# Performance work log

Hardware: AMD Instinct MI355X
Metric: run time of the kernel (lower is better)

## Reference

```python
import jax, jax.numpy as jnp
import numpy as np

B, L, D = 2, 2048, 2048
H, G, HD = 16, 4, 128
EPS = 1e-6
THETA_BASE = 10000.0


def setup_inputs() -> dict:
    key = jax.random.key(0)
    ks = jax.random.split(key, 5)
    x = jax.random.normal(ks[0], (B, L, D), jnp.float32)
    Wq = jax.random.normal(ks[1], (D, H * HD), jnp.float32) * 0.02
    Wk = jax.random.normal(ks[2], (D, G * HD), jnp.float32) * 0.02
    Wv = jax.random.normal(ks[3], (D, G * HD), jnp.float32) * 0.02
    Wo = jax.random.normal(ks[4], (H * HD, D), jnp.float32) * 0.02
    q_scale = jnp.ones((HD,), jnp.float32)
    k_scale = jnp.ones((HD,), jnp.float32)
    # Well-formed RoPE tables of shape [L, HD] (duplicated-half layout expected by apply_rope)
    inv_freq = 1.0 / (THETA_BASE ** (jnp.arange(0, HD // 2, dtype=jnp.float32) * 2.0 / HD))  # [HD/2]
    angles = jnp.arange(L, dtype=jnp.float32)[:, None] * inv_freq[None, :]  # [L, HD/2]
    angles = jnp.concatenate([angles, angles], axis=1)  # [L, HD]
    cos = jnp.cos(angles)
    sin = jnp.sin(angles)
    # Causal mask: True = masked (matches masked_fill(mask, -inf))
    mask = jnp.triu(jnp.ones((L, L), dtype=bool), k=1)
    return {"x": x, "Wq": Wq, "Wk": Wk, "Wv": Wv, "Wo": Wo,
            "q_scale": q_scale, "k_scale": k_scale, "cos": cos, "sin": sin, "mask": mask}


def _rmsnorm(x, scale):
    var = jnp.mean(x * x, axis=-1, keepdims=True)
    return x * jax.lax.rsqrt(var + EPS) * scale


def _rope(x, cos, sin):
    # x: [B, h, L, HD]; cos/sin: [L, HD]
    hd = x.shape[-1]
    x1, x2 = x[..., : hd // 2], x[..., hd // 2 :]
    rotated = jnp.concatenate([-x2, x1], axis=-1)
    return x * cos[None, None] + rotated * sin[None, None]


def reference(x, Wq, Wk, Wv, Wo, q_scale, k_scale, cos, sin, mask):
    b, l, _ = x.shape
    q = (x @ Wq).reshape(b, l, H, HD).transpose(0, 2, 1, 3)  # [B,H,L,HD]
    k = (x @ Wk).reshape(b, l, G, HD).transpose(0, 2, 1, 3)  # [B,G,L,HD]
    v = (x @ Wv).reshape(b, l, G, HD).transpose(0, 2, 1, 3)
    q = _rmsnorm(q, q_scale)
    k = _rmsnorm(k, k_scale)
    q = _rope(q, cos, sin)
    k = _rope(k, cos, sin)
    gs = H // G
    k = jnp.repeat(k, gs, axis=1)  # [B,H,L,HD]
    v = jnp.repeat(v, gs, axis=1)
    scores = jnp.einsum('bhqd,bhkd->bhqk', q, k)
    scores = jnp.where(mask, -jnp.inf, scores)
    # NB: faithful to the source's unusual scaling by head_dim**2 (not sqrt)
    w = jax.nn.softmax(scores / float(HD ** 2), axis=-1)
    out = jnp.einsum('bhqk,bhkd->bhqd', w, v).transpose(0, 2, 1, 3).reshape(b, l, H * HD)
    return out @ Wo
```

## Files before the change

kernel.cpp:

```cpp
#include <hip/hip_runtime.h>
#include <math.h>

#define SEQ 2048
#define DMODEL 2048
#define NHQ 16
#define NHK 4

typedef __attribute__((ext_vector_type(8))) short short8;
typedef __attribute__((ext_vector_type(8))) unsigned short ushort8;
typedef __attribute__((ext_vector_type(4))) float floatx4;

#define AS1 __attribute__((address_space(1)))
#define AS3 __attribute__((address_space(3)))

__device__ __forceinline__ unsigned short f2bf(float f) {
  unsigned int u = __builtin_bit_cast(unsigned int, f);
  u += 0x7fffu + ((u >> 16) & 1u);
  return (unsigned short)(u >> 16);
}
__device__ __forceinline__ float bf2f(unsigned short s) {
  unsigned int u = ((unsigned int)s) << 16;
  return __builtin_bit_cast(float, u);
}

__global__ __launch_bounds__(256) void prep(const float* __restrict__ x,
                                            const float* __restrict__ Wq,
                                            const float* __restrict__ Wk,
                                            const float* __restrict__ Wv,
                                            const float* __restrict__ Wo,
                                            unsigned short* __restrict__ x_bf,
                                            unsigned short* __restrict__ wqkv_t,
                                            unsigned short* __restrict__ wo_t) {
  const int z = blockIdx.z;
  const int tx = threadIdx.x, ty = threadIdx.y;
  const int tid = ty * 32 + tx;
  if (z == 3) {
    const size_t base = ((size_t)(blockIdx.y * 64 + blockIdx.x)) * 4096 + (size_t)tid * 16;
    const float4 v0 = *(const float4*)(x + base);
    const float4 v1 = *(const float4*)(x + base + 4);
    const float4 v2 = *(const float4*)(x + base + 8);
    const float4 v3 = *(const float4*)(x + base + 12);
    ushort8 w0, w1;
    w0[0] = f2bf(v0.x); w0[1] = f2bf(v0.y); w0[2] = f2bf(v0.z); w0[3] = f2bf(v0.w);
    w0[4] = f2bf(v1.x); w0[5] = f2bf(v1.y); w0[6] = f2bf(v1.z); w0[7] = f2bf(v1.w);
    w1[0] = f2bf(v2.x); w1[1] = f2bf(v2.y); w1[2] = f2bf(v2.z); w1[3] = f2bf(v2.w);
    w1[4] = f2bf(v3.x); w1[5] = f2bf(v3.y); w1[6] = f2bf(v3.z); w1[7] = f2bf(v3.w);
    *(ushort8*)(x_bf + base) = w0;
    *(ushort8*)(x_bf + base + 8) = w1;
    return;
  }
  int bx = blockIdx.x;
  const float* in;
  unsigned short* out;
  int C;
  const int R = 2048;
  if (z == 0)      { in = Wq; out = wqkv_t;                          C = 2048; }
  else if (z == 1) { in = Wo; out = wo_t;                            C = 2048; }
  else {
    if (bx < 16)      { in = Wk; out = wqkv_t + (size_t)2048 * 2048; C = 512; }
    else if (bx < 32) { in = Wv; out = wqkv_t + (size_t)2560 * 2048; C = 512; bx -= 16; }
    else return;
  }
  __shared__ float tile[32][65];
  const int c0 = bx * 32, r0 = blockIdx.y * 64;
#pragma unroll
  for (int j = 0; j < 8; ++j)
    tile[tx][ty + j * 8] = in[(size_t)(r0 + ty + j * 8) * C + c0 + tx];
  __syncthreads();
  const int c = tid >> 3;
  const int l8 = tid & 7;
  ushort8 w;
#pragma unroll
  for (int u = 0; u < 8; ++u) w[u] = f2bf(tile[c][l8 * 8 + u]);
  *(ushort8*)(out + (size_t)(c0 + c) * R + r0 + l8 * 8) = w;
}

#define PBAR() do { __builtin_amdgcn_sched_barrier(0); __builtin_amdgcn_s_barrier(); \
                    __builtin_amdgcn_sched_barrier(0); } while (0)
#define KWAIT(deep) do { if (deep) asm volatile("s_waitcnt vmcnt(8)" ::: "memory"); \
                         else      asm volatile("s_waitcnt vmcnt(0)" ::: "memory"); } while (0)

__device__ __forceinline__ void mfma_q(floatx4 (&ac)[4][4],
                                       const short8 (&a)[4], const short8 (&b)[4]) {
#pragma unroll
  for (int i = 0; i < 4; ++i)
#pragma unroll
    for (int j = 0; j < 4; ++j)
      ac[i][j] = __builtin_amdgcn_mfma_f32_16x16x32_bf16(a[i], b[j], ac[i][j], 0, 0, 0);
}

__device__ __forceinline__ void ld4(short8 (&v)[4], const unsigned short* p) {
#pragma unroll
  for (int i = 0; i < 4; ++i) v[i] = *(const short8*)(p + i * 512);
}

__device__ __forceinline__ void stg_half(const unsigned short* src0,
                                         unsigned short* dst_uniform) {
  __builtin_amdgcn_global_load_lds((const AS1 void*)src0,
                                   (AS3 void*)dst_uniform, 16, 0, 0);
  __builtin_amdgcn_global_load_lds((const AS1 void*)(src0 + (size_t)128 * 2048),
                                   (AS3 void*)(dst_uniform + 4096), 16, 0, 0);
}

__device__ __forceinline__ void kloop256(const unsigned short* __restrict__ A,
                                         const unsigned short* __restrict__ Bt,
                                         unsigned short* ldsA, unsigned short* ldsB,
                                         int bm, int bn, int tid,
                                         floatx4 (&accL)[4][4], floatx4 (&accH)[4][4]) {
  const int wave = tid >> 6;
  const int lane = tid & 63;
  const int m15 = lane & 15;
  const int quad = lane >> 4;
  const int wr = wave >> 2;
  const int wcol = wave & 3;

  const int srow = tid >> 2;
  const int csrc = ((tid & 3) ^ (srow & 3)) * 8;
  const unsigned short* gA = A + (size_t)(bm + srow) * 2048 + csrc;
  const unsigned short* gB = Bt + (size_t)(bn + srow) * 2048 + csrc;
  const int wslot = wave * 512;

  const int aoff = (wr * 128 + m15) * 32 + (quad ^ (m15 & 3)) * 8;
  const int boff = (wcol * 64 + m15) * 32 + (quad ^ (m15 & 3)) * 8;

  stg_half(gA + 0,  ldsA + wslot);
  stg_half(gB + 0,  ldsB + wslot);
  stg_half(gA + 32, ldsA + 8192 + wslot);
  stg_half(gB + 32, ldsB + 8192 + wslot);
  stg_half(gA + 64, ldsA + 16384 + wslot);
  stg_half(gB + 64, ldsB + 16384 + wslot);
  asm volatile("s_waitcnt vmcnt(0)" ::: "memory");
  __builtin_amdgcn_s_barrier();
  __builtin_amdgcn_sched_barrier(0);

  const int NK = 32;
  short8 af[4], bv[4];
  for (int t = 0; t < NK; ++t) {
    const int d = t & 1;
    unsigned short* Ab0 = ldsA + d * 16384;
    unsigned short* Bb0 = ldsB + d * 16384;
    unsigned short* Aalt = ldsA + (d ^ 1) * 16384;
    unsigned short* Balt = ldsB + (d ^ 1) * 16384;
    const bool st1 = (t + 1 < NK), st2 = (t + 2 < NK);
    const int k1 = (t + 1) * 64 + 32;
    const int k2 = (t + 2) * 64;

    ld4(af, Ab0 + aoff);
    ld4(bv, Bb0 + boff);
    if (st1) stg_half(gA + k1, Aalt + 8192 + wslot);
    PBAR();
    __builtin_amdgcn_s_setprio(1);
    mfma_q(accL, af, bv);
    __builtin_amdgcn_s_setprio(0);
    PBAR();

    ld4(af, Ab0 + aoff + 2048);
    if (st1) stg_half(gB + k1, Balt + 8192 + wslot);
    PBAR();
    __builtin_amdgcn_s_setprio(1);
    mfma_q(accH, af, bv);
    __builtin_amdgcn_s_setprio(0);
    KWAIT(st2);
    PBAR();

    ld4(af, Ab0 + 8192 + aoff);
    ld4(bv, Bb0 + 8192 + boff);
    if (st2) stg_half(gA + k2, Ab0 + wslot);
    PBAR();
    __builtin_amdgcn_s_setprio(1);
    mfma_q(accL, af, bv);
    __builtin_amdgcn_s_setprio(0);
    PBAR();

    ld4(af, Ab0 + 8192 + aoff + 2048);
    if (st2) stg_half(gB + k2, Bb0 + wslot);
    PBAR();
    __builtin_amdgcn_s_setprio(1);
    mfma_q(accH, af, bv);
    __builtin_amdgcn_s_setprio(0);
    KWAIT(st2);
    PBAR();
  }
}

__global__ __launch_bounds__(512, 2) void gemm_qkv_fused(const unsigned short* __restrict__ A,
                                                         const unsigned short* __restrict__ Bt,
                                                         unsigned short* __restrict__ qout,
                                                         unsigned short* __restrict__ kout,
                                                         unsigned short* __restrict__ vout,
                                                         const float* __restrict__ q_scale,
                                                         const float* __restrict__ k_scale,
                                                         const float* __restrict__ cosb,
                                                         const float* __restrict__ sinb) {
  __shared__ unsigned short lds[65536];
  unsigned short* ldsA = lds;
  unsigned short* ldsB = lds + 32768;

  const int tid = threadIdx.x;
  const int wave = tid >> 6;
  const int lane = tid & 63;
  const int m15 = lane & 15;
  const int quad = lane >> 4;
  const int wr = wave >> 2;
  const int wcol = wave & 3;
  const int bxn = blockIdx.x;
  const int bm = blockIdx.y * 256;
  const int bn = bxn * 256;

  floatx4 accL[4][4], accH[4][4];
#pragma unroll
  for (int i = 0; i < 4; ++i)
#pragma unroll
    for (int j = 0; j < 4; ++j) {
      accL[i][j] = (floatx4){0.f, 0.f, 0.f, 0.f};
      accH[i][j] = (floatx4){0.f, 0.f, 0.f, 0.f};
    }

  kloop256(A, Bt, ldsA, ldsB, bm, bn, tid, accL, accH);

  unsigned short* epi = lds;
  const int b = bm >> 11;
  const int l_base = bm & (SEQ - 1);
  const int t64 = tid & 63;

  for (int c = 0; c < 2; ++c) {
    __syncthreads();
    if ((wcol >> 1) == c) {
      const int colb = (wcol & 1) * 64;
#pragma unroll
      for (int i = 0; i < 4; ++i)
#pragma unroll
        for (int j = 0; j < 4; ++j)
#pragma unroll
          for (int r = 0; r < 4; ++r) {
            epi[(wr * 128 + i * 16 + quad * 4 + r) * 129 + colb + j * 16 + m15] =
                f2bf(accL[i][j][r]);
            epi[(wr * 128 + 64 + i * 16 + quad * 4 + r) * 129 + colb + j * 16 + m15] =
                f2bf(accH[i][j][r]);
          }
    }
    __syncthreads();

    const int hh = 2 * bxn + c;
    if (hh < 20) {
      const float* scale = (hh < NHQ) ? q_scale : k_scale;
      unsigned short* dstbase = (hh < NHQ)
          ? qout + ((size_t)(b * NHQ + hh) * SEQ + l_base) * 128
          : kout + ((size_t)(b * NHK + (hh - NHQ)) * SEQ + l_base) * 128;
      const float sc0 = scale[t64];
      const float sc1 = scale[t64 + 64];
#pragma unroll 4
      for (int rr = 0; rr < 32; ++rr) {
        const int row = wave * 32 + rr;
        const float v0 = bf2f(epi[row * 129 + t64]);
        const float v1 = bf2f(epi[row * 129 + t64 + 64]);
        float ss = v0 * v0 + v1 * v1;
#pragma unroll
        for (int m = 1; m < 64; m <<= 1) ss += __shfl_xor(ss, m);
        const float r = rsqrtf(ss * (1.0f / 128.0f) + 1e-6f);
        const int l = l_base + row;
        const float c0v = cosb[(size_t)l * 128 + t64];
        const float s0 = sinb[(size_t)l * 128 + t64];
        const float c1v = cosb[(size_t)l * 128 + t64 + 64];
        const float s1 = sinb[(size_t)l * 128 + t64 + 64];
        const float a0 = v0 * r * sc0;
        const float a1 = v1 * r * sc1;
        unsigned short* dst = dstbase + (size_t)row * 128;
        dst[t64]      = f2bf(a0 * c0v - a1 * s0);
        dst[t64 + 64] = f2bf(a1 * c1v + a0 * s1);
      }
    } else {
      const int g = hh - 20;
      unsigned short* vbase = vout + (size_t)(b * NHK + g) * 128 * SEQ + l_base;
#pragma unroll 4
      for (int dd = 0; dd < 16; ++dd) {
        const int d = wave * 16 + dd;
        unsigned short* dst = vbase + (size_t)d * SEQ;
        dst[t64]       = epi[t64 * 129 + d];
        dst[t64 + 64]  = epi[(t64 + 64) * 129 + d];
        dst[t64 + 128] = epi[(t64 + 128) * 129 + d];
        dst[t64 + 192] = epi[(t64 + 192) * 129 + d];
      }
    }
  }
}

__global__ __launch_bounds__(512, 2) void gemm_bf16_f32(const unsigned short* __restrict__ A,
                                                        const unsigned short* __restrict__ Bt,
                                                        float* __restrict__ C,
                                                        int M, int N, int K) {
  __shared__ unsigned short lds[65536];
  unsigned short* ldsA = lds;
  unsigned short* ldsB = lds + 32768;

  const int tid = threadIdx.x;
  const int wave = tid >> 6;
  const int lane = tid & 63;
  const int m15 = lane & 15;
  const int quad = lane >> 4;
  const int wr = wave >> 2;
  const int wcol = wave & 3;
  const int bm = blockIdx.y * 256;
  const int bn = blockIdx.x * 256;

  floatx4 accL[4][4], accH[4][4];
#pragma unroll
  for (int i = 0; i < 4; ++i)
#pragma unroll
    for (int j = 0; j < 4; ++j) {
      accL[i][j] = (floatx4){0.f, 0.f, 0.f, 0.f};
      accH[i][j] = (floatx4){0.f, 0.f, 0.f, 0.f};
    }

  kloop256(A, Bt, ldsA, ldsB, bm, bn, tid, accL, accH);

#pragma unroll
  for (int i = 0; i < 4; ++i)
#pragma unroll
    for (int j = 0; j < 4; ++j)
#pragma unroll
      for (int r = 0; r < 4; ++r) {
        const int col = bn + wcol * 64 + j * 16 + m15;
        C[(size_t)(bm + wr * 128 + i * 16 + quad * 4 + r) * N + col] = accL[i][j][r];
        C[(size_t)(bm + wr * 128 + 64 + i * 16 + quad * 4 + r) * N + col] = accH[i][j][r];
      }
}

__global__ __launch_bounds__(256, 4) void attn_mfma(const unsigned short* __restrict__ qb,
                                                    const unsigned short* __restrict__ kb,
                                                    const unsigned short* __restrict__ vtb,
                                                    unsigned short* __restrict__ o) {
  __shared__ unsigned short Ks[64 * 128];
  __shared__ unsigned short Vs[128 * 64];
  unsigned short* Ps = Ks;

  const int tid = threadIdx.x;
  const int wave = tid >> 6;
  const int lane = tid & 63;
  const int m15 = lane & 15;
  const int quad = lane >> 4;
  const int bh = blockIdx.x;
  const int b = bh >> 4;
  const int h = bh & 15;
  const int g = h >> 2;
  const int q0 = ((int)gridDim.y - 1 - (int)blockIdx.y) * 64;

  const unsigned short* qhead = qb + (size_t)bh * SEQ * 128;
  const unsigned short* khead = kb + (size_t)(b * NHK + g) * SEQ * 128;
  const unsigned short* vthead = vtb + (size_t)(b * NHK + g) * 128 * SEQ;

  short8 qf[4];
  {
    const unsigned short* qp = qhead + (size_t)(q0 + wave * 16 + m15) * 128 + quad * 8;
#pragma unroll
    for (int ks = 0; ks < 4; ++ks) qf[ks] = *(const short8*)(qp + ks * 32);
  }

  floatx4 acc_o[8];
#pragma unroll
  for (int n = 0; n < 8; ++n) acc_o[n] = (floatx4){0.f, 0.f, 0.f, 0.f};
  float l_lane[4] = {0.f, 0.f, 0.f, 0.f};
  const float inv_scale = 1.0f / 16384.0f;

  for (int j0 = 0; j0 <= q0; j0 += 64) {
#pragma unroll
    for (int t = 0; t < 4; ++t) {
      const int r = wave * 16 + t * 4 + (lane >> 4);
      const int cg = (lane & 15) ^ (r & 15);
      const unsigned short* src = khead + (size_t)(j0 + r) * 128 + cg * 8;
      __builtin_amdgcn_global_load_lds(
          (const AS1 void*)src,
          (AS3 void*)&Ks[(wave * 16 + t * 4) * 128], 16, 0, 0);
    }
#pragma unroll
    for (int t = 0; t < 4; ++t) {
      const int d = wave * 32 + t * 8 + (lane >> 3);
      const int cg = (lane & 7) ^ (d & 7);
      const unsigned short* src = vthead + (size_t)d * SEQ + j0 + cg * 8;
      __builtin_amdgcn_global_load_lds(
          (const AS1 void*)src,
          (AS3 void*)&Vs[(wave * 32 + t * 8) * 64], 16, 0, 0);
    }
    __syncthreads();

    floatx4 acc_s[4];
#pragma unroll
    for (int n = 0; n < 4; ++n) acc_s[n] = (floatx4){0.f, 0.f, 0.f, 0.f};
#pragma unroll
    for (int ks = 0; ks < 4; ++ks) {
#pragma unroll
      for (int n = 0; n < 4; ++n) {
        const short8 bfrag = *(const short8*)&Ks[(n * 16 + m15) * 128 + (((ks * 4 + quad) ^ m15) * 8)];
        acc_s[n] = __builtin_amdgcn_mfma_f32_16x16x32_bf16(qf[ks], bfrag, acc_s[n], 0, 0, 0);
      }
    }
    __syncthreads();

    if (j0 == q0) {
      const int row_g = wave * 16 + quad * 4;
#pragma unroll
      for (int n = 0; n < 4; ++n) {
        const int col = n * 16 + m15;
#pragma unroll
        for (int rg = 0; rg < 4; ++rg) {
          float p = (col > row_g + rg) ? 0.0f : __expf(acc_s[n][rg] * inv_scale);
          l_lane[rg] += p;
          Ps[(wave * 16 + quad * 4 + rg) * 72 + n * 16 + m15] = f2bf(p);
        }
      }
    } else {
#pragma unroll
      for (int n = 0; n < 4; ++n) {
#pragma unroll
        for (int rg = 0; rg < 4; ++rg) {
          const float p = __expf(acc_s[n][rg] * inv_scale);
          l_lane[rg] += p;
          Ps[(wave * 16 + quad * 4 + rg) * 72 + n * 16 + m15] = f2bf(p);
        }
      }
    }

#pragma unroll
    for (int kk = 0; kk < 2; ++kk) {
      const short8 a = *(const short8*)&Ps[(wave * 16 + m15) * 72 + kk * 32 + quad * 8];
#pragma unroll
      for (int n = 0; n < 8; ++n) {
        const short8 bfrag = *(const short8*)&Vs[(n * 16 + m15) * 64 + (((kk * 4 + quad) ^ (m15 & 7)) * 8)];
        acc_o[n] = __builtin_amdgcn_mfma_f32_16x16x32_bf16(a, bfrag, acc_o[n], 0, 0, 0);
      }
    }
    __syncthreads();
  }

#pragma unroll
  for (int rg = 0; rg < 4; ++rg) {
    float l = l_lane[rg];
    l += __shfl_xor(l, 1);
    l += __shfl_xor(l, 2);
    l += __shfl_xor(l, 4);
    l += __shfl_xor(l, 8);
    const float invl = 1.0f / l;
    const size_t row = (size_t)(b * SEQ + q0 + wave * 16 + quad * 4 + rg);
#pragma unroll
    for (int n = 0; n < 8; ++n)
      o[row * DMODEL + h * 128 + n * 16 + m15] = f2bf(acc_o[n][rg] * invl);
  }
}

extern "C" void kernel_launch(void* const* d_in, const int* in_sizes, int n_in,
                              void* d_out, int out_size, void* d_ws, size_t ws_size,
                              hipStream_t stream) {
  const float* x       = (const float*)d_in[0];
  const float* Wq      = (const float*)d_in[1];
  const float* Wk      = (const float*)d_in[2];
  const float* Wv      = (const float*)d_in[3];
  const float* Wo      = (const float*)d_in[4];
  const float* q_scale = (const float*)d_in[5];
  const float* k_scale = (const float*)d_in[6];
  const float* cosb    = (const float*)d_in[7];
  const float* sinb    = (const float*)d_in[8];
  float* out = (float*)d_out;

  char* w = (char*)d_ws;
  unsigned short* x_bf    = (unsigned short*)w;
  unsigned short* wqkv_t  = (unsigned short*)(w + 16777216);
  unsigned short* q_bf    = (unsigned short*)(w + 29360128);
  unsigned short* k_bf    = (unsigned short*)(w + 46137344);
  unsigned short* vt      = (unsigned short*)(w + 50331648);
  unsigned short* wo_t    = (unsigned short*)(w + 54525952);
  unsigned short* attn_bf = (unsigned short*)(w + 62914560);

  prep<<<dim3(64, 32, 4), dim3(32, 8), 0, stream>>>(x, Wq, Wk, Wv, Wo, x_bf, wqkv_t, wo_t);

  gemm_qkv_fused<<<dim3(12, 16), 512, 0, stream>>>(x_bf, wqkv_t, q_bf, k_bf, vt,
                                                   q_scale, k_scale, cosb, sinb);

  attn_mfma<<<dim3(2 * NHQ, SEQ / 64), 256, 0, stream>>>(q_bf, k_bf, vt, attn_bf);

  gemm_bf16_f32<<<dim3(2048 / 256, 4096 / 256), 512, 0, stream>>>(
      attn_bf, wo_t, out, 4096, 2048, 2048);
}
```

Before: 332.5 us.

## Shrink output GEMM tile to 128x256 and change LDS swizzle pattern

The output projection GEMM moves from 256x256 tiles to 128x256 tiles with its own single-accumulator k-loop, which doubles the grid from 128 to 256 blocks so that more of the device's compute units get work. LDS use drops, and the vmcnt wait depth is adjusted to the smaller staging count. The LDS XOR swizzle used by both the shared kloop and the new loop now keys on different row bits, aiming to reduce bank conflicts. In exchange, each block gets less operand reuse, so B-matrix traffic rises.

```diff
diff --git a/kernel.cpp b/kernel.cpp
--- a/kernel.cpp
+++ b/kernel.cpp
@@ -77,8 +77,10 @@
 
 #define PBAR() do { __builtin_amdgcn_sched_barrier(0); __builtin_amdgcn_s_barrier(); \
                     __builtin_amdgcn_sched_barrier(0); } while (0)
-#define KWAIT(deep) do { if (deep) asm volatile("s_waitcnt vmcnt(8)" ::: "memory"); \
-                         else      asm volatile("s_waitcnt vmcnt(0)" ::: "memory"); } while (0)
+#define KWAIT8(deep) do { if (deep) asm volatile("s_waitcnt vmcnt(8)" ::: "memory"); \
+                          else      asm volatile("s_waitcnt vmcnt(0)" ::: "memory"); } while (0)
+#define KWAIT6(deep) do { if (deep) asm volatile("s_waitcnt vmcnt(6)" ::: "memory"); \
+                          else      asm volatile("s_waitcnt vmcnt(0)" ::: "memory"); } while (0)
 
 __device__ __forceinline__ void mfma_q(floatx4 (&ac)[4][4],
                                        const short8 (&a)[4], const short8 (&b)[4]) {
@@ -100,6 +102,11 @@
                                    (AS3 void*)dst_uniform, 16, 0, 0);
   __builtin_amdgcn_global_load_lds((const AS1 void*)(src0 + (size_t)128 * 2048),
                                    (AS3 void*)(dst_uniform + 4096), 16, 0, 0);
+}
+__device__ __forceinline__ void stg_halfA(const unsigned short* src0,
+                                          unsigned short* dst_uniform) {
+  __builtin_amdgcn_global_load_lds((const AS1 void*)src0,
+                                   (AS3 void*)dst_uniform, 16, 0, 0);
 }
 
 __device__ __forceinline__ void kloop256(const unsigned short* __restrict__ A,
@@ -115,13 +122,14 @@
   const int wcol = wave & 3;
 
   const int srow = tid >> 2;
-  const int csrc = ((tid & 3) ^ (srow & 3)) * 8;
+  const int csrc = ((tid & 3) ^ ((tid >> 3) & 3)) * 8;
   const unsigned short* gA = A + (size_t)(bm + srow) * 2048 + csrc;
   const unsigned short* gB = Bt + (size_t)(bn + srow) * 2048 + csrc;
   const int wslot = wave * 512;
 
-  const int aoff = (wr * 128 + m15) * 32 + (quad ^ (m15 & 3)) * 8;
-  const int boff = (wcol * 64 + m15) * 32 + (quad ^ (m15 & 3)) * 8;
+  const int rc = (quad ^ ((m15 >> 1) & 3)) * 8;
+  const int aoff = (wr * 128 + m15) * 32 + rc;
+  const int boff = (wcol * 64 + m15) * 32 + rc;
 
   stg_half(gA + 0,  ldsA + wslot);
   stg_half(gB + 0,  ldsB + wslot);
@@ -160,7 +168,7 @@
     __builtin_amdgcn_s_setprio(1);
     mfma_q(accH, af, bv);
     __builtin_amdgcn_s_setprio(0);
-    KWAIT(st2);
+    KWAIT8(st2);
     PBAR();
 
     ld4(af, Ab0 + 8192 + aoff);
@@ -178,7 +186,7 @@
     __builtin_amdgcn_s_setprio(1);
     mfma_q(accH, af, bv);
     __builtin_amdgcn_s_setprio(0);
-    KWAIT(st2);
+    KWAIT8(st2);
     PBAR();
   }
 }
@@ -289,9 +297,9 @@
                                                         const unsigned short* __restrict__ Bt,
                                                         float* __restrict__ C,
                                                         int M, int N, int K) {
-  __shared__ unsigned short lds[65536];
+  __shared__ unsigned short lds[49152];
   unsigned short* ldsA = lds;
-  unsigned short* ldsB = lds + 32768;
+  unsigned short* ldsB = lds + 16384;
 
   const int tid = threadIdx.x;
   const int wave = tid >> 6;
@@ -300,19 +308,69 @@
   const int quad = lane >> 4;
   const int wr = wave >> 2;
   const int wcol = wave & 3;
-  const int bm = blockIdx.y * 256;
+  const int bm = blockIdx.y * 128;
   const int bn = blockIdx.x * 256;
 
-  floatx4 accL[4][4], accH[4][4];
+  floatx4 acc[4][4];
 #pragma unroll
   for (int i = 0; i < 4; ++i)
 #pragma unroll
-    for (int j = 0; j < 4; ++j) {
-      accL[i][j] = (floatx4){0.f, 0.f, 0.f, 0.f};
-      accH[i][j] = (floatx4){0.f, 0.f, 0.f, 0.f};
-    }
-
-  kloop256(A, Bt, ldsA, ldsB, bm, bn, tid, accL, accH);
+    for (int j = 0; j < 4; ++j) acc[i][j] = (floatx4){0.f, 0.f, 0.f, 0.f};
+
+  const int srow = tid >> 2;
+  const int csrc = ((tid & 3) ^ ((tid >> 3) & 3)) * 8;
+  const unsigned short* gA = A + (size_t)(bm + srow) * 2048 + csrc;
+  const unsigned short* gB = Bt + (size_t)(bn + srow) * 2048 + csrc;
+  const int wslot = wave * 512;
+
+  const int rc = (quad ^ ((m15 >> 1) & 3)) * 8;
+  const int aoff = (wr * 64 + m15) * 32 + rc;
+  const int boff = (wcol * 64 + m15) * 32 + rc;
+
+  stg_halfA(gA + 0,  ldsA + wslot);
+  stg_half (gB + 0,  ldsB + wslot);
+  stg_halfA(gA + 32, ldsA + 4096 + wslot);
+  stg_half (gB + 32, ldsB + 8192 + wslot);
+  stg_halfA(gA + 64, ldsA + 8192 + wslot);
+  stg_half (gB + 64, ldsB + 16384 + wslot);
+  asm volatile("s_waitcnt vmcnt(0)" ::: "memory");
+  __builtin_amdgcn_s_barrier();
+  __builtin_amdgcn_sched_barrier(0);
+
+  const int NK = 32;
+  short8 af[4], bv[4];
+  for (int t = 0; t < NK; ++t) {
+    const int d = t & 1;
+    unsigned short* Ab = ldsA + d * 8192;
+    unsigned short* Bb = ldsB + d * 16384;
+    unsigned short* Aalt = ldsA + (d ^ 1) * 8192;
+    unsigned short* Balt = ldsB + (d ^ 1) * 16384;
+    const bool st1 = (t + 1 < NK), st2 = (t + 2 < NK);
+    const int k1 = (t + 1) * 64 + 32;
+    const int k2 = (t + 2) * 64;
+
+    ld4(af, Ab + aoff);
+    ld4(bv, Bb + boff);
+    if (st1) { stg_halfA(gA + k1, Aalt + 4096 + wslot);
+               stg_half (gB + k1, Balt + 8192 + wslot); }
+    PBAR();
+    __builtin_amdgcn_s_setprio(1);
+    mfma_q(acc, af, bv);
+    __builtin_amdgcn_s_setprio(0);
+    KWAIT6(st2);
+    PBAR();
+
+    ld4(af, Ab + 4096 + aoff);
+    ld4(bv, Bb + 8192 + boff);
+    if (st2) { stg_halfA(gA + k2, Ab + wslot);
+               stg_half (gB + k2, Bb + wslot); }
+    PBAR();
+    __builtin_amdgcn_s_setprio(1);
+    mfma_q(acc, af, bv);
+    __builtin_amdgcn_s_setprio(0);
+    KWAIT6(st2);
+    PBAR();
+  }
 
 #pragma unroll
   for (int i = 0; i < 4; ++i)
@@ -321,8 +379,7 @@
 #pragma unroll
       for (int r = 0; r < 4; ++r) {
         const int col = bn + wcol * 64 + j * 16 + m15;
-        C[(size_t)(bm + wr * 128 + i * 16 + quad * 4 + r) * N + col] = accL[i][j][r];
-        C[(size_t)(bm + wr * 128 + 64 + i * 16 + quad * 4 + r) * N + col] = accH[i][j][r];
+        C[(size_t)(bm + wr * 64 + i * 16 + quad * 4 + r) * N + col] = acc[i][j][r];
       }
 }
 
@@ -477,6 +534,6 @@
 
   attn_mfma<<<dim3(2 * NHQ, SEQ / 64), 256, 0, stream>>>(q_bf, k_bf, vt, attn_bf);
 
-  gemm_bf16_f32<<<dim3(2048 / 256, 4096 / 256), 512, 0, stream>>>(
+  gemm_bf16_f32<<<dim3(2048 / 256, 4096 / 128), 512, 0, stream>>>(
       attn_bf, wo_t, out, 4096, 2048, 2048);
 }
```

Measured after the change: 304.4 us. 1.09x faster.
